# Optimization experiments

Measured on AMD Instinct MI355X. Metric: run time of the kernel, lower is better.

## Reference

```python
import jax, jax.numpy as jnp
import numpy as np

B, T, C = 4, 4096, 1024
DIM_K, DIM_V = 64, 64


def setup_inputs() -> dict:
    key = jax.random.key(0)
    k1, k2, k3, k4, k5, k6 = jax.random.split(key, 6)
    q_embs = jax.random.normal(k1, (B, T, C), dtype=jnp.float32)
    k_embs = jax.random.normal(k2, (B, T, C), dtype=jnp.float32)
    v_embs = jax.random.normal(k3, (B, T, C), dtype=jnp.float32)
    # nn.Linear(C, dim) weights have shape (dim, C); y = x @ W.T
    s = 1.0 / np.sqrt(C)
    w_q = jax.random.uniform(k4, (DIM_K, C), jnp.float32, -s, s)
    w_k = jax.random.uniform(k5, (DIM_K, C), jnp.float32, -s, s)
    w_v = jax.random.uniform(k6, (DIM_V, C), jnp.float32, -s, s)
    return {"q_embs": q_embs, "k_embs": k_embs, "v_embs": v_embs,
            "w_q": w_q, "w_k": w_k, "w_v": w_v}


def reference(q_embs, k_embs, v_embs, w_q, w_k, w_v):
    Bv, Tv, Cv = v_embs.shape
    q = jnp.einsum('btc,kc->btk', q_embs, w_q)  # [B,T,dim_k]
    k = jnp.einsum('btc,kc->btk', k_embs, w_k)  # [B,T,dim_k]
    v = jnp.einsum('btc,vc->btv', v_embs, w_v)  # [B,T,dim_v]
    # NOTE: original scales by C**-0.5 (embedding dim), not dim_k**-0.5
    scores = jnp.einsum('bqk,bsk->bqs', q, k) * (Cv ** -0.5)  # [B,T,T]
    causal = jnp.tril(jnp.ones((Tv, Tv), dtype=bool))
    scores = jnp.where(causal, scores, -jnp.inf)
    wei = jax.nn.softmax(scores, axis=-1)
    return jnp.einsum('bqs,bsv->bqv', wei, v)  # [B,T,dim_v]
```

## Files before the change

kernel.cpp:

```cpp
#include <hip/hip_runtime.h>

#define TSEQ 4096
#define CDIM 1024
#define DHEAD 64

typedef __bf16 bf16x8 __attribute__((ext_vector_type(8)));
typedef float f32x4 __attribute__((ext_vector_type(4)));

#define KCHUNK 128
#define NCHUNK (CDIM / KCHUNK)

__global__ __launch_bounds__(256) void wconv_kernel(
    const float* __restrict__ wq, const float* __restrict__ wk,
    const float* __restrict__ wv, __bf16* __restrict__ Wb)
{
  const int t = blockIdx.x * 256 + threadIdx.x;
  const int idx = t * 8;
  const int pid = idx >> 16;
  const float* __restrict__ src = (pid == 0) ? wq : ((pid == 1) ? wk : wv);
  const int off = idx & 65535;
  f32x4 a = *(const f32x4*)(src + off);
  f32x4 b = *(const f32x4*)(src + off + 4);
  ushort4 lo, hi;
  lo.x = __builtin_bit_cast(unsigned short, (__bf16)a[0]);
  lo.y = __builtin_bit_cast(unsigned short, (__bf16)a[1]);
  lo.z = __builtin_bit_cast(unsigned short, (__bf16)a[2]);
  lo.w = __builtin_bit_cast(unsigned short, (__bf16)a[3]);
  hi.x = __builtin_bit_cast(unsigned short, (__bf16)b[0]);
  hi.y = __builtin_bit_cast(unsigned short, (__bf16)b[1]);
  hi.z = __builtin_bit_cast(unsigned short, (__bf16)b[2]);
  hi.w = __builtin_bit_cast(unsigned short, (__bf16)b[3]);
  *(ushort4*)(Wb + idx) = lo;
  *(ushort4*)(Wb + idx + 4) = hi;
}

__global__ __launch_bounds__(256) void proj_kernel(
    const float* __restrict__ qe, const float* __restrict__ ke,
    const float* __restrict__ ve, const __bf16* __restrict__ Wb,
    __bf16* __restrict__ Qo, __bf16* __restrict__ Ko, __bf16* __restrict__ Vto)
{
  const int pid = blockIdx.y;
  const float* __restrict__ emb = (pid == 0) ? qe : ((pid == 1) ? ke : ve);
  const __bf16* __restrict__ W = Wb + (size_t)pid * DHEAD * CDIM;

  const int wave = threadIdx.x >> 6;
  const int lane = threadIdx.x & 63;
  const int g = lane >> 4, c = lane & 15;
  const int m0 = blockIdx.x * 64 + wave * 16;

  const float* __restrict__ arow = emb + (size_t)(m0 + c) * CDIM + g * 8;
  const __bf16* __restrict__ wbase = W + (size_t)c * CDIM + g * 8;

  f32x4 acc[4];
#pragma unroll
  for (int n = 0; n < 4; ++n) acc[n] = (f32x4){0.f, 0.f, 0.f, 0.f};

  auto loadA = [&](f32x4* L, f32x4* H, int ch) {
#pragma unroll
    for (int ks = 0; ks < 4; ++ks) {
      const float* p = arow + ch * KCHUNK + ks * 32;
      L[ks] = *(const f32x4*)(p);
      H[ks] = *(const f32x4*)(p + 4);
    }
  };
  auto compute = [&](const f32x4* L, const f32x4* H, int ch) {
#pragma unroll
    for (int ks = 0; ks < 4; ++ks) {
      bf16x8 af;
      af[0] = (__bf16)L[ks][0];
      af[1] = (__bf16)L[ks][1];
      af[2] = (__bf16)L[ks][2];
      af[3] = (__bf16)L[ks][3];
      af[4] = (__bf16)H[ks][0];
      af[5] = (__bf16)H[ks][1];
      af[6] = (__bf16)H[ks][2];
      af[7] = (__bf16)H[ks][3];
      const __bf16* wp = wbase + ch * KCHUNK + ks * 32;
#pragma unroll
      for (int n = 0; n < 4; ++n) {
        bf16x8 wf = *(const bf16x8*)(wp + (size_t)n * 16 * CDIM);
        acc[n] = __builtin_amdgcn_mfma_f32_16x16x32_bf16(af, wf, acc[n], 0, 0, 0);
      }
    }
  };

  f32x4 L[3][4], H[3][4];
  loadA(L[0], H[0], 0);
  loadA(L[1], H[1], 1);
  loadA(L[2], H[2], 2);
#pragma unroll
  for (int ch = 0; ch < NCHUNK; ++ch) {
    compute(L[ch % 3], H[ch % 3], ch);
    if (ch + 3 < NCHUNK) loadA(L[ch % 3], H[ch % 3], ch + 3);
  }

  if (pid < 2) {
    __bf16* __restrict__ dst = (pid == 0) ? Qo : Ko;
#pragma unroll
    for (int n = 0; n < 4; ++n)
#pragma unroll
      for (int r = 0; r < 4; ++r)
        dst[(size_t)(m0 + g * 4 + r) * DHEAD + n * 16 + c] = (__bf16)acc[n][r];
  } else {
    const int t0 = m0 + g * 4;
    const int bb = t0 >> 12;
    const int tl = t0 & (TSEQ - 1);
#pragma unroll
    for (int n = 0; n < 4; ++n) {
      const int v = n * 16 + c;
      ushort4 pk;
      pk.x = __builtin_bit_cast(unsigned short, (__bf16)acc[n][0]);
      pk.y = __builtin_bit_cast(unsigned short, (__bf16)acc[n][1]);
      pk.z = __builtin_bit_cast(unsigned short, (__bf16)acc[n][2]);
      pk.w = __builtin_bit_cast(unsigned short, (__bf16)acc[n][3]);
      *(ushort4*)(Vto + ((size_t)bb * DHEAD + v) * TSEQ + tl) = pk;
    }
  }
}

#define NWAVE 8

__global__ __launch_bounds__(512) void attn_kernel(
    const __bf16* __restrict__ Q, const __bf16* __restrict__ K,
    const __bf16* __restrict__ Vt, float* __restrict__ out)
{
  __shared__ __bf16 Plds[NWAVE][16][72];
  __shared__ float Om[NWAVE][16][65];
  __shared__ float La[NWAVE][16];

  const int b = blockIdx.y;
  const int tile = (int)gridDim.x - 1 - (int)blockIdx.x;
  const int q0 = tile * 16;
  const int wave = threadIdx.x >> 6;
  const int lane = threadIdx.x & 63;
  const int g = lane >> 4, c = lane & 15;

  const __bf16* Qb = Q + (size_t)b * TSEQ * DHEAD;
  const __bf16* Kb = K + (size_t)b * TSEQ * DHEAD;
  const __bf16* Vb = Vt + (size_t)b * DHEAD * TSEQ;

  bf16x8 aq0 = *(const bf16x8*)(Qb + (size_t)(q0 + c) * DHEAD + g * 8);
  bf16x8 aq1 = *(const bf16x8*)(Qb + (size_t)(q0 + c) * DHEAD + 32 + g * 8);

  bf16x8 ones;
#pragma unroll
  for (int j = 0; j < 8; ++j) ones[j] = (__bf16)1.0f;

  f32x4 o[4];
#pragma unroll
  for (int n = 0; n < 4; ++n) o[n] = (f32x4){0.f, 0.f, 0.f, 0.f};
  f32x4 lacc = (f32x4){0.f, 0.f, 0.f, 0.f};

  const float kScale = 0.04508422f;
  const int nt = (q0 + 16 + 63) >> 6;

  for (int st = wave; st < nt; st += 2 * NWAVE) {
    const int s0A = st * 64;
    const int stB = st + NWAVE;
    const bool hasB = stB < nt;
    const int s0B = stB * 64;

    bf16x8 ka0[4], ka1[4], kb0[4], kb1[4];
#pragma unroll
    for (int n = 0; n < 4; ++n) {
      const __bf16* kp = Kb + (size_t)(s0A + n * 16 + c) * DHEAD + g * 8;
      ka0[n] = *(const bf16x8*)(kp);
      ka1[n] = *(const bf16x8*)(kp + 32);
    }
    if (hasB) {
#pragma unroll
      for (int n = 0; n < 4; ++n) {
        const __bf16* kp = Kb + (size_t)(s0B + n * 16 + c) * DHEAD + g * 8;
        kb0[n] = *(const bf16x8*)(kp);
        kb1[n] = *(const bf16x8*)(kp + 32);
      }
    }

    f32x4 sA[4];
#pragma unroll
    for (int n = 0; n < 4; ++n) {
      f32x4 z = (f32x4){0.f, 0.f, 0.f, 0.f};
      z = __builtin_amdgcn_mfma_f32_16x16x32_bf16(aq0, ka0[n], z, 0, 0, 0);
      sA[n] = __builtin_amdgcn_mfma_f32_16x16x32_bf16(aq1, ka1[n], z, 0, 0, 0);
    }
    bf16x8 va0[4], va1[4];
#pragma unroll
    for (int n = 0; n < 4; ++n) {
      const __bf16* vp = Vb + (size_t)(n * 16 + c) * TSEQ + s0A + g * 8;
      va0[n] = *(const bf16x8*)(vp);
      va1[n] = *(const bf16x8*)(vp + 32);
    }
#pragma unroll
    for (int n = 0; n < 4; ++n) {
      const int sidx = s0A + n * 16 + c;
#pragma unroll
      for (int r = 0; r < 4; ++r) {
        const int qidx = q0 + g * 4 + r;
        float p = (sidx <= qidx) ? __builtin_amdgcn_exp2f(sA[n][r] * kScale) : 0.f;
        Plds[wave][g * 4 + r][n * 16 + c] = (__bf16)p;
      }
    }

    f32x4 sB[4];
    bf16x8 vb0[4], vb1[4];
    if (hasB) {
#pragma unroll
      for (int n = 0; n < 4; ++n) {
        f32x4 z = (f32x4){0.f, 0.f, 0.f, 0.f};
        z = __builtin_amdgcn_mfma_f32_16x16x32_bf16(aq0, kb0[n], z, 0, 0, 0);
        sB[n] = __builtin_amdgcn_mfma_f32_16x16x32_bf16(aq1, kb1[n], z, 0, 0, 0);
      }
#pragma unroll
      for (int n = 0; n < 4; ++n) {
        const __bf16* vp = Vb + (size_t)(n * 16 + c) * TSEQ + s0B + g * 8;
        vb0[n] = *(const bf16x8*)(vp);
        vb1[n] = *(const bf16x8*)(vp + 32);
      }
    }

    bf16x8 p0A = *(const bf16x8*)(&Plds[wave][c][g * 8]);
    bf16x8 p1A = *(const bf16x8*)(&Plds[wave][c][32 + g * 8]);
    lacc = __builtin_amdgcn_mfma_f32_16x16x32_bf16(p0A, ones, lacc, 0, 0, 0);
    lacc = __builtin_amdgcn_mfma_f32_16x16x32_bf16(p1A, ones, lacc, 0, 0, 0);

    if (hasB) {
#pragma unroll
      for (int n = 0; n < 4; ++n) {
        const int sidx = s0B + n * 16 + c;
#pragma unroll
        for (int r = 0; r < 4; ++r) {
          const int qidx = q0 + g * 4 + r;
          float p = (sidx <= qidx) ? __builtin_amdgcn_exp2f(sB[n][r] * kScale) : 0.f;
          Plds[wave][g * 4 + r][n * 16 + c] = (__bf16)p;
        }
      }
    }

#pragma unroll
    for (int n = 0; n < 4; ++n) {
      o[n] = __builtin_amdgcn_mfma_f32_16x16x32_bf16(p0A, va0[n], o[n], 0, 0, 0);
      o[n] = __builtin_amdgcn_mfma_f32_16x16x32_bf16(p1A, va1[n], o[n], 0, 0, 0);
    }

    if (hasB) {
      bf16x8 p0B = *(const bf16x8*)(&Plds[wave][c][g * 8]);
      bf16x8 p1B = *(const bf16x8*)(&Plds[wave][c][32 + g * 8]);
      lacc = __builtin_amdgcn_mfma_f32_16x16x32_bf16(p0B, ones, lacc, 0, 0, 0);
      lacc = __builtin_amdgcn_mfma_f32_16x16x32_bf16(p1B, ones, lacc, 0, 0, 0);
#pragma unroll
      for (int n = 0; n < 4; ++n) {
        o[n] = __builtin_amdgcn_mfma_f32_16x16x32_bf16(p0B, vb0[n], o[n], 0, 0, 0);
        o[n] = __builtin_amdgcn_mfma_f32_16x16x32_bf16(p1B, vb1[n], o[n], 0, 0, 0);
      }
    }
  }

#pragma unroll
  for (int n = 0; n < 4; ++n)
#pragma unroll
    for (int r = 0; r < 4; ++r)
      Om[wave][g * 4 + r][n * 16 + c] = o[n][r];
  if (c == 0) {
#pragma unroll
    for (int r = 0; r < 4; ++r) La[wave][g * 4 + r] = lacc[r];
  }
  __syncthreads();

  const int tid = threadIdx.x;
  const int q = tid >> 5;
  const int c2 = (tid & 31) * 2;
  float l = 0.f;
#pragma unroll
  for (int w = 0; w < NWAVE; ++w) l += La[w][q];
  float s0 = 0.f, s1 = 0.f;
#pragma unroll
  for (int w = 0; w < NWAVE; ++w) {
    s0 += Om[w][q][c2];
    s1 += Om[w][q][c2 + 1];
  }
  const float inv = 1.0f / l;
  float2 r;
  r.x = s0 * inv;
  r.y = s1 * inv;
  *(float2*)(out + ((size_t)b * TSEQ + q0 + q) * DHEAD + c2) = r;
}

extern "C" void kernel_launch(void* const* d_in, const int* in_sizes, int n_in,
                              void* d_out, int out_size, void* d_ws, size_t ws_size,
                              hipStream_t stream) {
  const float* qe = (const float*)d_in[0];
  const float* ke = (const float*)d_in[1];
  const float* ve = (const float*)d_in[2];
  const float* wq = (const float*)d_in[3];
  const float* wk = (const float*)d_in[4];
  const float* wv = (const float*)d_in[5];

  __bf16* Qw  = (__bf16*)d_ws;
  __bf16* Kw  = Qw + (size_t)4 * TSEQ * DHEAD;
  __bf16* Vtw = Kw + (size_t)4 * TSEQ * DHEAD;
  __bf16* Wb  = Vtw + (size_t)4 * TSEQ * DHEAD;

  wconv_kernel<<<dim3(96), dim3(256), 0, stream>>>(wq, wk, wv, Wb);

  dim3 g1(4 * TSEQ / 64, 3), b1(256);
  proj_kernel<<<g1, b1, 0, stream>>>(qe, ke, ve, Wb, Qw, Kw, Vtw);

  dim3 g2(TSEQ / 16, 4), b2(512);
  attn_kernel<<<g2, b2, 0, stream>>>(Qw, Kw, Vtw, (float*)d_out);
}
```

Baseline: 291.6 us.

## Stage projection activations through LDS with async global_load_lds double buffering

New measurement: 279.8 us. -4.1%, faster.

```diff
diff --git a/kernel.cpp b/kernel.cpp
--- a/kernel.cpp
+++ b/kernel.cpp
@@ -6,9 +6,6 @@
 
 typedef __bf16 bf16x8 __attribute__((ext_vector_type(8)));
 typedef float f32x4 __attribute__((ext_vector_type(4)));
-
-#define KCHUNK 128
-#define NCHUNK (CDIM / KCHUNK)
 
 __global__ __launch_bounds__(256) void wconv_kernel(
     const float* __restrict__ wq, const float* __restrict__ wk,
@@ -34,11 +31,16 @@
   *(ushort4*)(Wb + idx + 4) = hi;
 }
 
+#define PKCH 64
+#define PNCH (CDIM / PKCH)
+
 __global__ __launch_bounds__(256) void proj_kernel(
     const float* __restrict__ qe, const float* __restrict__ ke,
     const float* __restrict__ ve, const __bf16* __restrict__ Wb,
     __bf16* __restrict__ Qo, __bf16* __restrict__ Ko, __bf16* __restrict__ Vto)
 {
+  __shared__ __align__(16) float Abuf[2][64 * PKCH];
+
   const int pid = blockIdx.y;
   const float* __restrict__ emb = (pid == 0) ? qe : ((pid == 1) ? ke : ve);
   const __bf16* __restrict__ W = Wb + (size_t)pid * DHEAD * CDIM;
@@ -46,52 +48,72 @@
   const int wave = threadIdx.x >> 6;
   const int lane = threadIdx.x & 63;
   const int g = lane >> 4, c = lane & 15;
-  const int m0 = blockIdx.x * 64 + wave * 16;
-
-  const float* __restrict__ arow = emb + (size_t)(m0 + c) * CDIM + g * 8;
-  const __bf16* __restrict__ wbase = W + (size_t)c * CDIM + g * 8;
+  const int bm0 = blockIdx.x * 64;
+  const int m0 = bm0 + wave * 16;
+
+  size_t gsrc[4];
+  int lofs[4];
+#pragma unroll
+  for (int j = 0; j < 4; ++j) {
+    const int row = (wave * 4 + j) * 4 + (lane >> 4);
+    const int colb = ((lane & 15) << 4) ^ ((row & 7) << 4);
+    gsrc[j] = (size_t)(bm0 + row) * CDIM + (colb >> 2);
+    lofs[j] = (wave * 4 + j) * 256;
+  }
+
+  const int arow = wave * 16 + c;
+  const int aswz = (arow & 7) << 4;
+  int ra0[2], ra1[2];
+#pragma unroll
+  for (int ks = 0; ks < 2; ++ks) {
+    const int ncol = ks * 128 + g * 32;
+    ra0[ks] = arow * 256 + ((ncol) ^ aswz);
+    ra1[ks] = arow * 256 + ((ncol + 16) ^ aswz);
+  }
 
   f32x4 acc[4];
 #pragma unroll
   for (int n = 0; n < 4; ++n) acc[n] = (f32x4){0.f, 0.f, 0.f, 0.f};
 
-  auto loadA = [&](f32x4* L, f32x4* H, int ch) {
-#pragma unroll
-    for (int ks = 0; ks < 4; ++ks) {
-      const float* p = arow + ch * KCHUNK + ks * 32;
-      L[ks] = *(const f32x4*)(p);
-      H[ks] = *(const f32x4*)(p + 4);
+  auto stage = [&](int buf, int ch) {
+    const float* __restrict__ eb = emb + (size_t)ch * PKCH;
+    float* lb = &Abuf[buf][0];
+#pragma unroll
+    for (int j = 0; j < 4; ++j) {
+      __builtin_amdgcn_global_load_lds(
+          (const __attribute__((address_space(1))) void*)(uintptr_t)(eb + gsrc[j]),
+          (__attribute__((address_space(3))) void*)(unsigned)(uintptr_t)(lb + lofs[j]),
+          16, 0, 0);
     }
   };
-  auto compute = [&](const f32x4* L, const f32x4* H, int ch) {
-#pragma unroll
-    for (int ks = 0; ks < 4; ++ks) {
+
+  stage(0, 0);
+  __syncthreads();
+
+  for (int ch = 0; ch < PNCH; ++ch) {
+    if (ch + 1 < PNCH) stage((ch + 1) & 1, ch + 1);
+    const char* base = (const char*)&Abuf[ch & 1][0];
+    const __bf16* __restrict__ wp = W + (size_t)ch * PKCH + g * 8;
+#pragma unroll
+    for (int ks = 0; ks < 2; ++ks) {
+      f32x4 lo = *(const f32x4*)(base + ra0[ks]);
+      f32x4 hi = *(const f32x4*)(base + ra1[ks]);
       bf16x8 af;
-      af[0] = (__bf16)L[ks][0];
-      af[1] = (__bf16)L[ks][1];
-      af[2] = (__bf16)L[ks][2];
-      af[3] = (__bf16)L[ks][3];
-      af[4] = (__bf16)H[ks][0];
-      af[5] = (__bf16)H[ks][1];
-      af[6] = (__bf16)H[ks][2];
-      af[7] = (__bf16)H[ks][3];
-      const __bf16* wp = wbase + ch * KCHUNK + ks * 32;
-#pragma unroll
-      for (int n = 0; n < 4; ++n) {
-        bf16x8 wf = *(const bf16x8*)(wp + (size_t)n * 16 * CDIM);
+      af[0] = (__bf16)lo[0];
+      af[1] = (__bf16)lo[1];
+      af[2] = (__bf16)lo[2];
+      af[3] = (__bf16)lo[3];
+      af[4] = (__bf16)hi[0];
+      af[5] = (__bf16)hi[1];
+      af[6] = (__bf16)hi[2];
+      af[7] = (__bf16)hi[3];
+#pragma unroll
+      for (int n = 0; n < 4; ++n) {
+        bf16x8 wf = *(const bf16x8*)(wp + (size_t)(n * 16 + c) * CDIM + ks * 32);
         acc[n] = __builtin_amdgcn_mfma_f32_16x16x32_bf16(af, wf, acc[n], 0, 0, 0);
       }
     }
-  };
-
-  f32x4 L[3][4], H[3][4];
-  loadA(L[0], H[0], 0);
-  loadA(L[1], H[1], 1);
-  loadA(L[2], H[2], 2);
-#pragma unroll
-  for (int ch = 0; ch < NCHUNK; ++ch) {
-    compute(L[ch % 3], H[ch % 3], ch);
-    if (ch + 3 < NCHUNK) loadA(L[ch % 3], H[ch % 3], ch + 3);
+    __syncthreads();
   }
 
   if (pid < 2) {
```
